# Kernel tuning notes

Measured on AMD Instinct MI355X. Metric: run time of the kernel, lower is better.

The kernel has to match this reference:

```python
import jax, jax.numpy as jnp
import numpy as np

TAU = 20.0
TH = 1.0
TAU_THETA = 50.0
THETA_INC = 0.5
REFRAC_STEPS = 5
K = 10.0  # surrogate sigmoid sharpness
B, L = 65536, 400


def setup_inputs() -> dict:
    key = jax.random.key(0)
    I = jax.random.normal(key, (B, L), dtype=jnp.float32)
    return {"I": I}


def _lif_forward(I):
    Bn, Ln = I.shape
    dt = I.dtype

    def step(carry, I_t):
        v, theta, ref = carry
        # Euler membrane update: v += -v/tau + I_t
        v = v + (-v / TAU + I_t)
        can_spike = (ref == 0)
        x = v - theta
        s_soft = jax.nn.sigmoid(K * x) * can_spike.astype(dt)
        s_hard = ((x >= 0.0) & can_spike).astype(dt)
        # straight-through: value = s_hard, gradient flows through s_soft
        s = jax.lax.stop_gradient(s_hard - s_soft) + s_soft
        ref = jnp.where(s_hard > 0, jnp.int32(REFRAC_STEPS), jnp.maximum(ref - 1, 0))
        # reset uses detached spike (multiplier is a constant wrt grad)
        v = v * (1.0 - jax.lax.stop_gradient(s))
        # adaptive threshold: decay to base + bump on hard spike
        theta = theta - (theta - TH) / TAU_THETA + THETA_INC * s_hard
        return (v, theta, ref), (s, s_hard)

    init = (jnp.zeros((Bn,), dt), jnp.full((Bn,), TH, dt), jnp.zeros((Bn,), jnp.int32))
    _, (spikes_t, hard_t) = jax.lax.scan(step, init, jnp.swapaxes(I, 0, 1))
    spikes = jnp.swapaxes(spikes_t, 0, 1)       # [B, L]
    hard_spikes = jnp.swapaxes(hard_t, 0, 1)    # [B, L]
    return spikes, hard_spikes


def _soft_lat(spikes):
    Ln = spikes.shape[1]
    time = jnp.arange(Ln, dtype=spikes.dtype)
    w = spikes / (spikes.sum(axis=1, keepdims=True) + 1e-6)
    return (w * time).sum(axis=1)


def reference(I):
    spikes, hard_spikes = _lif_forward(I)
    fired = hard_spikes > 0.5
    has_spike = jnp.any(fired, axis=1)
    first_idx = jnp.argmax(fired, axis=1)
    hard_latency = jnp.where(has_spike, first_idx, I.shape[1]).astype(jnp.int64)
    soft_latency = _soft_lat(spikes)
    return spikes, hard_latency, soft_latency
```

## Files before the change

### kernel.cpp

```cpp
#include <hip/hip_runtime.h>


constexpr int Bsz  = 65536;
constexpr int Lsz  = 400;
constexpr int ROWS = 64;
constexpr int TC   = 40;
constexpr int NCH  = Lsz / TC;
constexpr int PW   = 2 * TC;
constexpr int STRIDE = PW + 1;
constexpr int V4   = TC / 4;
constexpr int PV4  = PW / 4;

typedef float floatx4 __attribute__((ext_vector_type(4)));

__global__ __launch_bounds__(ROWS)
void lif_kernel(const float* __restrict__ I, float* __restrict__ out)
{
    __shared__ float tile[ROWS * STRIDE];

    const int tid = threadIdx.x;
    const int rb  = blockIdx.x * ROWS;
    const int row = rb + tid;

    const float* Irow = I   + (size_t)row * Lsz;
    float*       Sb   = out + (size_t)rb  * Lsz;

    float4 regA[V4], regB[V4];

    auto glb_load = [&](int ch, float4* rg) {
#pragma unroll
        for (int it = 0; it < V4; ++it)
            rg[it] = *reinterpret_cast<const float4*>(Irow + ch * TC + it * 4);
    };

    float v     = 0.0f;
    float theta = 1.0f;
    int   allow = 0;
    int   first = Lsz;
    float cnt   = 0.0f;
    float swt   = 0.0f;

    auto body = [&](const float4* rg, int t0, int off) {
        float* myrow = &tile[tid * STRIDE + off];
        const float* in = reinterpret_cast<const float*>(rg);
        float cnt_l = 0.0f, swt_l = 0.0f;
#pragma unroll
        for (int c = 0; c < TC; ++c) {
            const float It = in[c];
            v = __builtin_fmaf(v, 0.95f, It);
            const int t = t0 + c;
            const bool hard = (v >= theta) & (t >= allow);
            const float s   = hard ? 1.0f : 0.0f;
            v     = hard ? 0.0f : v;
            theta = __builtin_fmaf(theta, 0.98f, hard ? 0.52f : 0.02f);
            allow = hard ? (t + 6) : allow;
            myrow[c] = s;
            cnt_l += s;
            swt_l = __builtin_fmaf(s, (float)c, swt_l);
            first = hard ? min(first, t) : first;
        }
        swt = __builtin_fmaf(cnt_l, (float)t0, swt + swt_l);
        cnt += cnt_l;
    };

    auto store_pair = [&](int pair) {
#pragma unroll
        for (int it = 0; it < PV4; ++it) {
            const int idx = it * ROWS + tid;
            const int r   = idx / PV4;
            const int c4  = idx % PV4;
            const float* sp = &tile[r * STRIDE + c4 * 4];
            floatx4 vv = { sp[0], sp[1], sp[2], sp[3] };
            __builtin_nontemporal_store(vv,
                reinterpret_cast<floatx4*>(Sb + (size_t)r * Lsz + pair * PW + c4 * 4));
        }
    };

    glb_load(0, regA);
    glb_load(1, regB);

    for (int ch = 0; ch < NCH; ch += 2) {
        body(regA, ch * TC, 0);
        if (ch + 2 < NCH) glb_load(ch + 2, regA);
        body(regB, (ch + 1) * TC, TC);
        if (ch + 3 < NCH) glb_load(ch + 3, regB);
        store_pair(ch >> 1);
    }

    out[(size_t)Bsz * Lsz + row]       = (float)first;
    out[(size_t)Bsz * Lsz + Bsz + row] = swt / (cnt + 1e-6f);
}

extern "C" void kernel_launch(void* const* d_in, const int* in_sizes, int n_in,
                              void* d_out, int out_size, void* d_ws, size_t ws_size,
                              hipStream_t stream)
{
    const float* I = (const float*)d_in[0];
    float* out = (float*)d_out;
    lif_kernel<<<dim3(Bsz / ROWS), dim3(ROWS), 0, stream>>>(I, out);
}
```

Measured before the change: 38.00 us.

## Split block into producer and compute wavefronts with bit-packed spike staging

Each block now runs two wavefronts. One acts as a producer: it loads input chunks into double-buffered shared memory and expands bit-packed spikes into float stores. The other runs the serial LIF recurrence and records spikes as bits in 32-bit words. Count and weighted-time statistics are computed from those words with popcount. The aim is to overlap global memory traffic with the serial scan and to cut shared-memory volume. In exchange it adds per-chunk block barriers and doubles the threads per block, which could make the two wavefronts wait on each other.

```diff
diff --git a/kernel.cpp b/kernel.cpp
--- a/kernel.cpp
+++ b/kernel.cpp
@@ -5,90 +5,126 @@
 constexpr int Lsz  = 400;
 constexpr int ROWS = 64;
 constexpr int TC   = 40;
-constexpr int NCH  = Lsz / TC;
-constexpr int PW   = 2 * TC;
-constexpr int STRIDE = PW + 1;
+constexpr int STRIDE = 41;
 constexpr int V4   = TC / 4;
-constexpr int PV4  = PW / 4;
 
 typedef float floatx4 __attribute__((ext_vector_type(4)));
 
-__global__ __launch_bounds__(ROWS)
+__device__ __forceinline__ int sumpos(unsigned int w) {
+    return __popc(w & 0xAAAAAAAAu) + (__popc(w & 0xCCCCCCCCu) << 1) +
+           (__popc(w & 0xF0F0F0F0u) << 2) + (__popc(w & 0xFF00FF00u) << 3) +
+           (__popc(w & 0xFFFF0000u) << 4);
+}
+
+__global__ __launch_bounds__(2 * ROWS)
 void lif_kernel(const float* __restrict__ I, float* __restrict__ out)
 {
-    __shared__ float tile[ROWS * STRIDE];
+    __shared__ float in2[2][ROWS * STRIDE];
+    __shared__ unsigned int bits[2][ROWS * 4];
 
-    const int tid = threadIdx.x;
-    const int rb  = blockIdx.x * ROWS;
-    const int row = rb + tid;
+    const int tid  = threadIdx.x;
+    const int wv   = tid >> 6;
+    const int lane = tid & 63;
+    const int rb   = blockIdx.x * ROWS;
 
-    const float* Irow = I   + (size_t)row * Lsz;
-    float*       Sb   = out + (size_t)rb  * Lsz;
+    if (wv == 1) {
+        const float* Irow = I + (size_t)(rb + lane) * Lsz;
+        float* Sb = out + (size_t)rb * Lsz;
+        float4 rg[V4];
 
-    float4 regA[V4], regB[V4];
+        auto issue = [&](int ch) {
+#pragma unroll
+            for (int it = 0; it < V4; ++it)
+                rg[it] = *reinterpret_cast<const float4*>(Irow + ch * TC + it * 4);
+        };
+        auto put = [&](int buf) {
+            const float* f = reinterpret_cast<const float*>(rg);
+            float* dst = &in2[buf][lane * STRIDE];
+#pragma unroll
+            for (int c = 0; c < TC; ++c) dst[c] = f[c];
+        };
+        auto expand_half = [&](int pair, int half) {
+            const unsigned int* bl = bits[pair & 1];
+#pragma unroll
+            for (int q = 0; q < 10; ++q) {
+                const int it  = half * 10 + q;
+                const int idx = it * ROWS + lane;
+                const int r   = idx / 20;
+                const int c4  = idx % 20;
+                const unsigned int word = bl[r * 4 + (c4 >> 3)];
+                const int bb = (c4 & 7) * 4;
+                floatx4 vv = { (float)((word >> (bb + 0)) & 1u),
+                               (float)((word >> (bb + 1)) & 1u),
+                               (float)((word >> (bb + 2)) & 1u),
+                               (float)((word >> (bb + 3)) & 1u) };
+                __builtin_nontemporal_store(vv,
+                    reinterpret_cast<floatx4*>(Sb + (size_t)r * Lsz + pair * 80 + c4 * 4));
+            }
+        };
 
-    auto glb_load = [&](int ch, float4* rg) {
+        issue(0); put(0); issue(1);
+        __syncthreads();
+        for (int pr = 0; pr < 5; ++pr) {
+            const int ch = 2 * pr;
+            put(1);
+            if (ch + 2 < 10) issue(ch + 2);
+            if (pr >= 1) expand_half(pr - 1, 0);
+            __syncthreads();
+            if (ch + 2 < 10) put(0);
+            if (ch + 3 < 10) issue(ch + 3);
+            if (pr >= 1) expand_half(pr - 1, 1);
+            __syncthreads();
+        }
+        expand_half(4, 0); expand_half(4, 1);
+    } else {
+        float v = 0.0f, theta = 1.0f;
+        int allow = 0, first = Lsz;
+        int cnt_i = 0, swt_i = 0;
+        unsigned int w0, w1, w2;
+
+        auto scan_chunk = [&](int buf, int t0, int gb) {
+            const float* src = &in2[buf][lane * STRIDE];
+            float rg[TC];
 #pragma unroll
-        for (int it = 0; it < V4; ++it)
-            rg[it] = *reinterpret_cast<const float4*>(Irow + ch * TC + it * 4);
-    };
+            for (int c = 0; c < TC; ++c) rg[c] = src[c];
+#pragma unroll
+            for (int c = 0; c < TC; ++c) {
+                v = __builtin_fmaf(v, 0.95f, rg[c]);
+                const int t = t0 + c;
+                const bool hard = (v >= theta) & (t >= allow);
+                v     = hard ? 0.0f : v;
+                theta = __builtin_fmaf(theta, 0.98f, hard ? 0.52f : 0.02f);
+                allow = hard ? (t + 6) : allow;
+                const int cg = gb + c;
+                const unsigned int m = hard ? (1u << (cg & 31)) : 0u;
+                if (cg < 32) w0 |= m; else if (cg < 64) w1 |= m; else w2 |= m;
+            }
+        };
 
-    float v     = 0.0f;
-    float theta = 1.0f;
-    int   allow = 0;
-    int   first = Lsz;
-    float cnt   = 0.0f;
-    float swt   = 0.0f;
-
-    auto body = [&](const float4* rg, int t0, int off) {
-        float* myrow = &tile[tid * STRIDE + off];
-        const float* in = reinterpret_cast<const float*>(rg);
-        float cnt_l = 0.0f, swt_l = 0.0f;
-#pragma unroll
-        for (int c = 0; c < TC; ++c) {
-            const float It = in[c];
-            v = __builtin_fmaf(v, 0.95f, It);
-            const int t = t0 + c;
-            const bool hard = (v >= theta) & (t >= allow);
-            const float s   = hard ? 1.0f : 0.0f;
-            v     = hard ? 0.0f : v;
-            theta = __builtin_fmaf(theta, 0.98f, hard ? 0.52f : 0.02f);
-            allow = hard ? (t + 6) : allow;
-            myrow[c] = s;
-            cnt_l += s;
-            swt_l = __builtin_fmaf(s, (float)c, swt_l);
-            first = hard ? min(first, t) : first;
+        __syncthreads();
+        for (int pr = 0; pr < 5; ++pr) {
+            w0 = w1 = w2 = 0u;
+            scan_chunk(0, 2 * pr * TC, 0);
+            __syncthreads();
+            scan_chunk(1, (2 * pr + 1) * TC, TC);
+            const int tp = pr * 80;
+            const int p0 = __popc(w0), p1 = __popc(w1), p2 = __popc(w2);
+            const int cp = p0 + p1 + p2;
+            cnt_i += cp;
+            swt_i += tp * cp + sumpos(w0) + sumpos(w1) + 32 * p1 +
+                     sumpos(w2) + 64 * p2;
+            const int cand = w0 ? tp + (__ffs(w0) - 1)
+                           : w1 ? tp + 32 + (__ffs(w1) - 1)
+                           : w2 ? tp + 64 + (__ffs(w2) - 1) : Lsz;
+            first = min(first, cand);
+            *reinterpret_cast<uint4*>(&bits[pr & 1][lane * 4]) =
+                make_uint4(w0, w1, w2, 0u);
+            __syncthreads();
         }
-        swt = __builtin_fmaf(cnt_l, (float)t0, swt + swt_l);
-        cnt += cnt_l;
-    };
-
-    auto store_pair = [&](int pair) {
-#pragma unroll
-        for (int it = 0; it < PV4; ++it) {
-            const int idx = it * ROWS + tid;
-            const int r   = idx / PV4;
-            const int c4  = idx % PV4;
-            const float* sp = &tile[r * STRIDE + c4 * 4];
-            floatx4 vv = { sp[0], sp[1], sp[2], sp[3] };
-            __builtin_nontemporal_store(vv,
-                reinterpret_cast<floatx4*>(Sb + (size_t)r * Lsz + pair * PW + c4 * 4));
-        }
-    };
-
-    glb_load(0, regA);
-    glb_load(1, regB);
-
-    for (int ch = 0; ch < NCH; ch += 2) {
-        body(regA, ch * TC, 0);
-        if (ch + 2 < NCH) glb_load(ch + 2, regA);
-        body(regB, (ch + 1) * TC, TC);
-        if (ch + 3 < NCH) glb_load(ch + 3, regB);
-        store_pair(ch >> 1);
+        const int row = rb + lane;
+        out[(size_t)Bsz * Lsz + row]       = (float)first;
+        out[(size_t)Bsz * Lsz + Bsz + row] = (float)swt_i / ((float)cnt_i + 1e-6f);
     }
-
-    out[(size_t)Bsz * Lsz + row]       = (float)first;
-    out[(size_t)Bsz * Lsz + Bsz + row] = swt / (cnt + 1e-6f);
 }
 
 extern "C" void kernel_launch(void* const* d_in, const int* in_sizes, int n_in,
@@ -97,5 +133,5 @@
 {
     const float* I = (const float*)d_in[0];
     float* out = (float*)d_out;
-    lif_kernel<<<dim3(Bsz / ROWS), dim3(ROWS), 0, stream>>>(I, out);
+    lif_kernel<<<dim3(Bsz / ROWS), dim3(2 * ROWS), 0, stream>>>(I, out);
 }
```

Result: no change. 37.74 us (-0.7%).
